# Kernel optimization log

Measured on AMD Instinct MI355X. Metric: run time of the kernel, lower is better.

The kernel has to match this reference:

```python
import jax, jax.numpy as jnp
import numpy as np

B, N, T, M, DIM = 4, 4096, 16, 64, 1024
HEADS, DH = 8, 64
INNER = HEADS * DH  # 512
KV = T * M          # 1024


def setup_inputs() -> dict:
    key = jax.random.key(0)
    ks = jax.random.split(key, 8)
    x = jax.random.normal(ks[0], (B, N, DIM), jnp.float32)
    media = jax.random.normal(ks[1], (B, T, M, DIM), jnp.float32)
    # sparse media markers so cumsum(text_time) stays within [0, T]
    media_locations = jax.random.uniform(ks[2], (B, N)) < (T / N)
    ln_scale = jnp.ones((DIM,), jnp.float32)
    ln_bias = jnp.zeros((DIM,), jnp.float32)
    s_in = DIM ** -0.5
    Wq = jax.random.normal(ks[3], (DIM, INNER), jnp.float32) * s_in
    Wk = jax.random.normal(ks[4], (DIM, INNER), jnp.float32) * s_in
    Wv = jax.random.normal(ks[5], (DIM, INNER), jnp.float32) * s_in
    Wo = jax.random.normal(ks[6], (INNER, DIM), jnp.float32) * (INNER ** -0.5)
    return dict(x=x, media=media, media_locations=media_locations,
                ln_scale=ln_scale, ln_bias=ln_bias, Wq=Wq, Wk=Wk, Wv=Wv, Wo=Wo)


def reference(x, media, media_locations, ln_scale, ln_bias, Wq, Wk, Wv, Wo):
    scale = DH ** -0.5
    # LayerNorm(eps=1e-5)
    mu = jnp.mean(x, axis=-1, keepdims=True)
    var = jnp.mean((x - mu) ** 2, axis=-1, keepdims=True)
    xn = (x - mu) / jnp.sqrt(var + 1e-5) * ln_scale + ln_bias

    q = xn @ Wq                                   # [b, n, inner]
    media_f = media.reshape(B, KV, DIM)           # b (t m) d
    k = media_f @ Wk                              # [b, kv, inner]
    v = media_f @ Wv

    q = q.reshape(B, N, HEADS, DH).transpose(0, 2, 1, 3) * scale  # b h n d
    k = k.reshape(B, KV, HEADS, DH).transpose(0, 2, 1, 3)         # b h kv d
    v = v.reshape(B, KV, HEADS, DH).transpose(0, 2, 1, 3)

    sim = jnp.einsum('bhid,bhjd->bhij', q, k)     # [b, h, n, kv]

    # media-location mask: each text token attends only to its immediately
    # preceding media item (only_attend_immediate_media=True -> eq)
    text_time = jnp.cumsum(media_locations.astype(jnp.int32), axis=-1)  # [b, n]
    media_time = jnp.repeat(jnp.arange(1, T + 1), M)                    # [kv]
    mask = text_time[:, None, :, None] == media_time[None, None, None, :]
    sim = jnp.where(mask, sim, -jnp.finfo(sim.dtype).max)

    attn = jax.nn.softmax(sim, axis=-1)  # stable (subtracts rowmax), same math
    # NOTE: the original's masked_fill_ of attn for media-less text tokens is a
    # no-op (return value discarded), faithfully omitted here.

    out = jnp.einsum('bhij,bhjd->bhid', attn, v)  # b h n d
    out = out.transpose(0, 2, 1, 3).reshape(B, N, INNER)
    return out @ Wo
```

## Files before the change

### kernel.cpp

```cpp
#include <hip/hip_runtime.h>

using u16 = unsigned short;
using uch = unsigned char;

typedef __bf16 bf16x8 __attribute__((ext_vector_type(8)));
typedef float f32x4 __attribute__((ext_vector_type(4)));

#define BATCH 4
#define SEQN 4096
#define TT 16
#define MM 64
#define DIM 1024
#define HEADS 8
#define DH 64
#define INNER 512
#define KVN 1024
#define NTOK (BATCH*SEQN)
#define MAXBLK 352

#define OFF_XN     ((size_t)0)
#define OFF_MEDIA  ((size_t)33554432)
#define OFF_Q      ((size_t)41943040)
#define OFF_KV     ((size_t)58720256)
#define OFF_AOUT   ((size_t)67108864)
#define OFF_WQT    ((size_t)83886080)
#define OFF_WKVT   ((size_t)84934656)
#define OFF_WOT    ((size_t)87031808)
#define OFF_VSUM   ((size_t)88145920)
#define OFF_FLAGS  ((size_t)88154112)
#define OFF_VT     ((size_t)88155136)
#define OFF_NBLK   ((size_t)92350464)
#define OFF_DESC   ((size_t)92351488)

__device__ __forceinline__ u16 f2bf(float f){
  unsigned int u = __float_as_uint(f);
  u += 0x7fffu + ((u >> 16) & 1u);
  return (u16)(u >> 16);
}
__device__ __forceinline__ float bf2f(u16 b){ return __uint_as_float(((unsigned int)b) << 16); }

__device__ __forceinline__ void async16(const u16* g, void* l){
  __builtin_amdgcn_global_load_lds((__attribute__((address_space(1))) void*)(g),
                                   (__attribute__((address_space(3))) void*)(l), 16, 0, 0);
}

__global__ __launch_bounds__(1024) void prep_kernel(const unsigned int* __restrict__ x,
                             const uch* __restrict__ loc, int* __restrict__ flags,
                             float* __restrict__ vsum, int4* __restrict__ desc,
                             int* __restrict__ nblk){
  __shared__ int cnt, nonz, sflags1;
  __shared__ int wsumS[4][4];
  __shared__ int sbound[4][19];
  __shared__ int gcnt[73];
  const int tid = threadIdx.x;
  if (tid == 0){ cnt = 0; nonz = 0; }
  if (tid < 76) sbound[tid/19][tid%19] = 4096;
  vsum[tid] = 0.f; vsum[1024 + tid] = 0.f;
  __syncthreads();
  if (tid < 256){
    int c = 0;
    #pragma unroll
    for (int t = 0; t < 4; ++t){
      unsigned int w = x[t*256 + tid];
      unsigned int e = (w >> 7) & 0xFFu;
      if (e >= 110u && e <= 140u) c++;
    }
    atomicAdd(&cnt, c);
  } else if (tid < 512){
    int tt = tid - 256;
    int nz = 0;
    #pragma unroll
    for (int t = 0; t < 16; ++t){
      int i = t*256 + tt;
      if ((i & 3) && loc[i]) nz++;
    }
    atomicAdd(&nonz, nz);
  }
  __syncthreads();
  if (tid == 0){
    flags[0] = (cnt > 512) ? 1 : 0;
    sflags1 = (nonz == 0) ? 1 : 0;
    flags[1] = sflags1;
  }
  __syncthreads();
  const int as32 = sflags1;
  const int b = tid >> 8, t8 = tid & 255;
  const int lane = tid & 63, wl = (tid >> 6) & 3;
  int v[16];
  if (as32){
    const int4* p = (const int4*)((const int*)loc + b*SEQN + t8*16);
    #pragma unroll
    for (int j = 0; j < 4; ++j){
      int4 q = p[j];
      v[j*4+0] = q.x != 0; v[j*4+1] = q.y != 0; v[j*4+2] = q.z != 0; v[j*4+3] = q.w != 0;
    }
  } else {
    const uchar4* p = (const uchar4*)(loc + b*SEQN + t8*16);
    #pragma unroll
    for (int j = 0; j < 4; ++j){
      uchar4 q = p[j];
      v[j*4+0] = q.x != 0; v[j*4+1] = q.y != 0; v[j*4+2] = q.z != 0; v[j*4+3] = q.w != 0;
    }
  }
  int tsum = 0;
  #pragma unroll
  for (int j = 0; j < 16; ++j) tsum += v[j];
  int s = tsum;
  #pragma unroll
  for (int o = 1; o < 64; o <<= 1){ int n2 = __shfl_up(s, o); if (lane >= o) s += n2; }
  if (lane == 63) wsumS[b][wl] = s;
  __syncthreads();
  int base = 0;
  for (int w2 = 0; w2 < wl; ++w2) base += wsumS[b][w2];
  int tt = base + s - tsum;
  #pragma unroll
  for (int j = 0; j < 16; ++j){
    if (v[j]){ tt++; if (tt <= 17) sbound[b][tt] = t8*16 + j; }
  }
  __syncthreads();
  if (tid < 72){
    int bb = tid/18, g = tid%18;
    int lo = (g == 0) ? 0 : sbound[bb][g];
    int hi = (g < 17) ? sbound[bb][g+1] : 4096;
    if (hi < lo) hi = lo;
    gcnt[tid] = (hi - lo + 63) >> 6;
  }
  __syncthreads();
  if (tid == 0){
    int acc = 0;
    for (int i = 0; i < 72; ++i){ int c2 = gcnt[i]; gcnt[i] = acc; acc += c2; }
    *nblk = acc;
  }
  __syncthreads();
  if (tid < 72){
    int bb = tid/18, g = tid%18;
    int lo = (g == 0) ? 0 : sbound[bb][g];
    int hi = (g < 17) ? sbound[bb][g+1] : 4096;
    if (hi < lo) hi = lo;
    int s2 = (g == 0 || g == 17) ? -1 : (g - 1);
    int n0 = gcnt[tid];
    for (int k = lo, j = 0; k < hi; k += 64, ++j){
      int4 d; d.x = bb; d.y = s2; d.z = bb*4096 + k; d.w = min(64, hi - k);
      desc[n0 + j] = d;
    }
  }
}

__global__ void wtrans_all_kernel(const void* __restrict__ Wq, const void* __restrict__ Wk,
                                  const void* __restrict__ Wv, const void* __restrict__ Wo,
                                  u16* __restrict__ WqT, u16* __restrict__ WkvT, u16* __restrict__ WoT,
                                  const int* __restrict__ flags){
  const int bf = flags[0];
  __shared__ float tile[32][33];
  int id = blockIdx.x;
  const void* in; u16* out; int K, N, bx, by;
  if (id < 512){       in = Wq; out = WqT;  K = DIM;   N = INNER; int l = id;        bx = l & 15; by = l >> 4; }
  else if (id < 1024){ in = Wk; out = WkvT; K = DIM;   N = INNER; int l = id - 512;  bx = l & 15; by = l >> 4; }
  else if (id < 1536){ in = Wv; out = WkvT + (size_t)512*1024; K = DIM; N = INNER; int l = id - 1024; bx = l & 15; by = l >> 4; }
  else {               in = Wo; out = WoT;  K = INNER; N = DIM;   int l = id - 1536; bx = l & 31; by = l >> 5; }
  int n0 = bx*32, k0 = by*32;
  int tx = threadIdx.x, ty = threadIdx.y;
  #pragma unroll
  for (int i = 0; i < 4; ++i){
    size_t idx = (size_t)(k0 + ty + i*8)*N + n0 + tx;
    tile[ty + i*8][tx] = bf ? bf2f(((const u16*)in)[idx]) : ((const float*)in)[idx];
  }
  __syncthreads();
  #pragma unroll
  for (int i = 0; i < 4; ++i)
    out[(size_t)(n0 + ty + i*8)*K + k0 + tx] = f2bf(tile[tx][ty + i*8]);
}

__global__ __launch_bounds__(256) void ln_cvt_kernel(const void* __restrict__ xp, const void* __restrict__ gp,
                          const void* __restrict__ bp, u16* __restrict__ xn,
                          const void* __restrict__ media, u16* __restrict__ medb,
                          const int* __restrict__ flags){
  const int bf = flags[0];
  const int tid = threadIdx.x;
  if ((int)blockIdx.x >= NTOK){
    size_t i = (size_t)(blockIdx.x - NTOK)*256 + tid;
    if (bf){
      ((ushort4*)medb)[i] = ((const ushort4*)media)[i];
    } else {
      float4 t = ((const float4*)media)[i];
      ushort4 o; o.x = f2bf(t.x); o.y = f2bf(t.y); o.z = f2bf(t.z); o.w = f2bf(t.w);
      ((ushort4*)medb)[i] = o;
    }
    return;
  }
  const int row = blockIdx.x;
  float v[4];
  if (bf){
    ushort4 t = ((const ushort4*)((const u16*)xp + (size_t)row*DIM))[tid];
    v[0]=bf2f(t.x); v[1]=bf2f(t.y); v[2]=bf2f(t.z); v[3]=bf2f(t.w);
  } else {
    float4 t = ((const float4*)((const float*)xp + (size_t)row*DIM))[tid];
    v[0]=t.x; v[1]=t.y; v[2]=t.z; v[3]=t.w;
  }
  float s = v[0]+v[1]+v[2]+v[3];
  float sq = v[0]*v[0]+v[1]*v[1]+v[2]*v[2]+v[3]*v[3];
  #pragma unroll
  for (int o = 32; o > 0; o >>= 1){ s += __shfl_down(s, o); sq += __shfl_down(sq, o); }
  __shared__ float ss[4], ssq[4];
  int wid = tid >> 6, lane = tid & 63;
  if (lane == 0){ ss[wid] = s; ssq[wid] = sq; }
  __syncthreads();
  s = ss[0]+ss[1]+ss[2]+ss[3]; sq = ssq[0]+ssq[1]+ssq[2]+ssq[3];
  float mean = s * (1.f/DIM);
  float rstd = rsqrtf(sq * (1.f/DIM) - mean*mean + 1e-5f);
  float g[4], bb[4];
  if (bf){
    ushort4 t1 = ((const ushort4*)gp)[tid]; ushort4 t2 = ((const ushort4*)bp)[tid];
    g[0]=bf2f(t1.x); g[1]=bf2f(t1.y); g[2]=bf2f(t1.z); g[3]=bf2f(t1.w);
    bb[0]=bf2f(t2.x); bb[1]=bf2f(t2.y); bb[2]=bf2f(t2.z); bb[3]=bf2f(t2.w);
  } else {
    float4 t1 = ((const float4*)gp)[tid]; float4 t2 = ((const float4*)bp)[tid];
    g[0]=t1.x; g[1]=t1.y; g[2]=t1.z; g[3]=t1.w;
    bb[0]=t2.x; bb[1]=t2.y; bb[2]=t2.z; bb[3]=t2.w;
  }
  ushort4 o;
  o.x = f2bf((v[0]-mean)*rstd*g[0] + bb[0]);
  o.y = f2bf((v[1]-mean)*rstd*g[1] + bb[1]);
  o.z = f2bf((v[2]-mean)*rstd*g[2] + bb[2]);
  o.w = f2bf((v[3]-mean)*rstd*g[3] + bb[3]);
  ((ushort4*)(xn + (size_t)row*DIM))[tid] = o;
}

__global__ __launch_bounds__(256) void gemm_kv(const u16* __restrict__ A, const u16* __restrict__ Bt,
                        u16* __restrict__ Cp, int M, int N, int K,
                        const int* __restrict__ flags, u16* __restrict__ vtp,
                        float* __restrict__ vsum){
  __shared__ u16 As[128*64];
  __shared__ u16 Bs[128*64];
  const int tid = threadIdx.x, wid = tid >> 6, lane = tid & 63;
  int flat = blockIdx.x + blockIdx.y*gridDim.x;
  int cpx = (gridDim.x*gridDim.y) >> 3;
  int wg = (flat & 7)*cpx + (flat >> 3);
  const int rn = wg % gridDim.x, rm = wg / gridDim.x;
  const int wr = wid >> 1, wc = wid & 1;
  const int lr = lane & 15, lg = lane >> 4;
  f32x4 acc[4][4] = {};
  const u16* Ab = A + (size_t)rm*128*K;
  const u16* Bb = Bt + (size_t)rn*128*K;
  for (int k0 = 0; k0 < K; k0 += 64){
    __syncthreads();
    #pragma unroll
    for (int t = 0; t < 4; ++t){
      int c = t*256 + tid;
      int row = c >> 3;
      int qs = (c & 7) ^ (row & 7);
      int ldsOff = (t*256 + wid*64) * 16;
      async16(Ab + (size_t)row*K + k0 + qs*8, (char*)As + ldsOff);
      async16(Bb + (size_t)row*K + k0 + qs*8, (char*)Bs + ldsOff);
    }
    __syncthreads();
    #pragma unroll
    for (int ks = 0; ks < 2; ++ks){
      bf16x8 af[4], bfr[4];
      #pragma unroll
      for (int m = 0; m < 4; ++m){
        int row = wr*64 + m*16 + lr;
        int q = (ks*4 + lg) ^ (row & 7);
        af[m] = *(const bf16x8*)((const char*)As + row*128 + (q << 4));
      }
      #pragma unroll
      for (int n = 0; n < 4; ++n){
        int row = wc*64 + n*16 + lr;
        int q = (ks*4 + lg) ^ (row & 7);
        bfr[n] = *(const bf16x8*)((const char*)Bs + row*128 + (q << 4));
      }
      #pragma unroll
      for (int m = 0; m < 4; ++m)
        #pragma unroll
        for (int n = 0; n < 4; ++n)
          acc[m][n] = __builtin_amdgcn_mfma_f32_16x16x32_bf16(af[m], bfr[n], acc[m][n], 0, 0, 0);
    }
  }
  const int batch = rm >> 3;
  #pragma unroll
  for (int n = 0; n < 4; ++n){
    int col = rn*128 + wc*64 + n*16 + lr;
    float psum = 0.f;
    #pragma unroll
    for (int m = 0; m < 4; ++m){
      int row0 = rm*128 + wr*64 + m*16 + lg*4;
      #pragma unroll
      for (int r = 0; r < 4; ++r){
        float v = acc[m][n][r];
        psum += v;
        size_t idx = (size_t)(row0 + r)*N + col;
        u16 bv = f2bf(v);
        Cp[idx] = bv;
        if (col >= 512){
          int row = row0 + r;
          int kvi = row & 1023;
          int s = kvi >> 6, rr = kvi & 63;
          vtp[((size_t)(((row >> 10)*16 + s)*512 + (col - 512)))*64 + rr] = bv;
        }
      }
    }
    if (col >= 512) atomicAdd(&vsum[batch*512 + (col - 512)], psum);
  }
}

template<int ROWS>
__device__ __forceinline__ void g8_stage(const u16* __restrict__ src, char* dst, int K, int t,
                                         int tid, int wid){
  #pragma unroll
  for (int i = 0; i < ROWS/64; ++i){
    int s_ = i*512 + tid;
    int row_ = s_ >> 3, g_ = s_ & 7;
    async16(src + (size_t)row_*K + t*64 + ((g_ ^ (row_ & 7)) << 3),
            dst + (size_t)(i*512 + wid*64)*16);
  }
}

template<int BN, int NT, int MODE>
__global__ __launch_bounds__(512, 2) void gemm8(const u16* __restrict__ A, const u16* __restrict__ Bt,
                        void* __restrict__ Cp, int Nglob, float alpha, const int* __restrict__ flags){
  constexpr int K = NT*64;
  constexpr int NREP = BN/64;
  __shared__ u16 As[2][256*64];
  __shared__ u16 Bs[2][BN*64];
  const int tid = threadIdx.x, wid = tid >> 6, lane = tid & 63;
  int flat = blockIdx.x + blockIdx.y*gridDim.x;
  int cpx = (gridDim.x*gridDim.y) >> 3;
  int wg = (flat & 7)*cpx + (flat >> 3);
  const int rn = wg % gridDim.x, rm = wg / gridDim.x;
  const int wr = wid >> 2, wc = wid & 3;
  const int lr = lane & 15, lg = lane >> 4;
  f32x4 acc[8][NREP] = {};
  const u16* Ab = A + (size_t)rm*256*K;
  const u16* Bb = Bt + (size_t)rn*BN*K;

  g8_stage<256>(Ab, (char*)As[0], K, 0, tid, wid);
  g8_stage<BN >(Bb, (char*)Bs[0], K, 0, tid, wid);
  __syncthreads();

  for (int t = 0; t < NT; ++t){
    const int cur = t & 1;
    const char* Acur = (const char*)As[cur];
    const char* Bcur = (const char*)Bs[cur];
    bf16x8 bfr[NREP][2];
    #pragma unroll
    for (int p = 0; p < 4; ++p){
      if (p == 0 && t + 1 < NT){
        g8_stage<256>(Ab, (char*)As[cur^1], K, t+1, tid, wid);
        g8_stage<BN >(Bb, (char*)Bs[cur^1], K, t+1, tid, wid);
      }
      bf16x8 af[2][2];
      #pragma unroll
      for (int i = 0; i < 2; ++i){
        int row = wr*128 + (2*p + i)*16 + lr;
        #pragma unroll
        for (int ks = 0; ks < 2; ++ks){
          int g = (ks*4 + lg) ^ (row & 7);
          af[i][ks] = *(const bf16x8*)(Acur + row*128 + g*16);
        }
      }
      if (p == 0){
        #pragma unroll
        for (int n = 0; n < NREP; ++n){
          int row = wc*(BN/4) + n*16 + lr;
          #pragma unroll
          for (int ks = 0; ks < 2; ++ks){
            int g = (ks*4 + lg) ^ (row & 7);
            bfr[n][ks] = *(const bf16x8*)(Bcur + row*128 + g*16);
          }
        }
      }
      __builtin_amdgcn_s_barrier();
      __builtin_amdgcn_s_setprio(1);
      #pragma unroll
      for (int i = 0; i < 2; ++i)
        #pragma unroll
        for (int n = 0; n < NREP; ++n)
          #pragma unroll
          for (int ks = 0; ks < 2; ++ks)
            acc[2*p + i][n] = __builtin_amdgcn_mfma_f32_16x16x32_bf16(af[i][ks], bfr[n][ks], acc[2*p + i][n], 0, 0, 0);
      __builtin_amdgcn_s_setprio(0);
      __builtin_amdgcn_s_barrier();
    }
    if (t + 1 < NT) __syncthreads();
  }

  const bool obf = (MODE == 0) || (flags[0] != 0);
  #pragma unroll
  for (int m = 0; m < 8; ++m){
    #pragma unroll
    for (int n = 0; n < NREP; ++n){
      int row0 = rm*256 + wr*128 + m*16 + lg*4;
      int col  = rn*BN + wc*(BN/4) + n*16 + lr;
      #pragma unroll
      for (int r = 0; r < 4; ++r){
        float v = acc[m][n][r] * alpha;
        size_t idx = (size_t)(row0 + r)*Nglob + col;
        if (obf) ((u16*)Cp)[idx] = f2bf(v);
        else     ((float*)Cp)[idx] = v;
      }
    }
  }
}

__global__ __launch_bounds__(256) void attn2_kernel(
    const u16* __restrict__ qb, const u16* __restrict__ kvb, const u16* __restrict__ vt,
    const int* __restrict__ nblk, const int4* __restrict__ desc,
    const float* __restrict__ vsum, u16* __restrict__ aout){
  __shared__ u16 Ks[64*64];
  __shared__ u16 Vs[64*64];
  __shared__ u16 Ps[4][16*72];
  if (blockIdx.x >= *nblk) return;
  const int4 d = desc[blockIdx.x];
  const int b = d.x, s = d.y, rowStart = d.z, cnt = d.w;
  const int h = blockIdx.y;
  const int tid = threadIdx.x, w = tid >> 6, lane = tid & 63;
  if (s < 0){
    const float inv = 1.f/1024.f;
    for (int idx = tid; idx < cnt*64; idx += 256){
      int slot = idx >> 6, c = h*64 + (idx & 63);
      aout[(size_t)(rowStart + slot)*512 + c] = f2bf(vsum[b*512 + c]*inv);
    }
    return;
  }
  const int lr = lane & 15, lg = lane >> 4;
  const size_t kbase = ((size_t)(b*1024 + s*64))*1024;
  const size_t vbase = ((size_t)(b*16 + s))*512*64;
  const int myslot = w*16 + lr;
  const size_t qrow = (size_t)(rowStart + min(myslot, cnt - 1))*512;
  #pragma unroll
  for (int t = 0; t < 2; ++t){
    int ci = t*256 + tid;
    int r = ci >> 3, q = ci & 7;
    int qs = (q ^ (r & 7)) << 3;
    async16(kvb + kbase + (size_t)r*1024 + h*64 + qs, (char*)Ks + ci*16);
    async16(vt + vbase + (size_t)(h*64 + r)*64 + qs, (char*)Vs + ci*16);
  }
  __syncthreads();
  bf16x8 qa0 = *(const bf16x8*)(qb + qrow + h*64 + lg*8);
  bf16x8 qa1 = *(const bf16x8*)(qb + qrow + h*64 + 32 + lg*8);
  f32x4 sv[4] = {};
  #pragma unroll
  for (int n = 0; n < 4; ++n){
    int row = n*16 + lr;
    int sl0 = (lg) ^ (row & 7);
    int sl1 = (4 + lg) ^ (row & 7);
    bf16x8 kb0 = *(const bf16x8*)((const char*)Ks + row*128 + sl0*16);
    sv[n] = __builtin_amdgcn_mfma_f32_16x16x32_bf16(qa0, kb0, sv[n], 0, 0, 0);
    bf16x8 kb1 = *(const bf16x8*)((const char*)Ks + row*128 + sl1*16);
    sv[n] = __builtin_amdgcn_mfma_f32_16x16x32_bf16(qa1, kb1, sv[n], 0, 0, 0);
  }
  float inv[4];
  #pragma unroll
  for (int r = 0; r < 4; ++r){
    float m = fmaxf(fmaxf(sv[0][r], sv[1][r]), fmaxf(sv[2][r], sv[3][r]));
    #pragma unroll
    for (int o = 1; o < 16; o <<= 1) m = fmaxf(m, __shfl_xor(m, o));
    float s0 = 0.f;
    #pragma unroll
    for (int n = 0; n < 4; ++n){ sv[n][r] = __expf(sv[n][r] - m); s0 += sv[n][r]; }
    #pragma unroll
    for (int o = 1; o < 16; o <<= 1) s0 += __shfl_xor(s0, o);
    inv[r] = 1.f / s0;
  }
  u16* pw = &Ps[w][0];
  #pragma unroll
  for (int n = 0; n < 4; ++n)
    #pragma unroll
    for (int r = 0; r < 4; ++r)
      pw[(4*lg + r)*72 + n*16 + lr] = f2bf(sv[n][r] * inv[r]);
  bf16x8 pa0 = *(const bf16x8*)((const char*)pw + lr*144 + lg*16);
  bf16x8 pa1 = *(const bf16x8*)((const char*)pw + lr*144 + 64 + lg*16);
  f32x4 ov[4] = {};
  #pragma unroll
  for (int n = 0; n < 4; ++n){
    int row = n*16 + lr;
    int sl0 = (lg) ^ (row & 7);
    int sl1 = (4 + lg) ^ (row & 7);
    bf16x8 vb0 = *(const bf16x8*)((const char*)Vs + row*128 + sl0*16);
    ov[n] = __builtin_amdgcn_mfma_f32_16x16x32_bf16(pa0, vb0, ov[n], 0, 0, 0);
    bf16x8 vb1 = *(const bf16x8*)((const char*)Vs + row*128 + sl1*16);
    ov[n] = __builtin_amdgcn_mfma_f32_16x16x32_bf16(pa1, vb1, ov[n], 0, 0, 0);
  }
  #pragma unroll
  for (int r = 0; r < 4; ++r){
    int slot = w*16 + 4*lg + r;
    if (slot < cnt){
      size_t orow = (size_t)(rowStart + slot)*512 + h*64;
      #pragma unroll
      for (int n = 0; n < 4; ++n)
        aout[orow + n*16 + lr] = f2bf(ov[n][r]);
    }
  }
}

extern "C" void kernel_launch(void* const* d_in, const int* in_sizes, int n_in,
                              void* d_out, int out_size, void* d_ws, size_t ws_size,
                              hipStream_t stream){
  const void* x      = d_in[0];
  const void* media  = d_in[1];
  const void* mloc   = d_in[2];
  const void* ln_g   = d_in[3];
  const void* ln_b   = d_in[4];
  const void* Wq     = d_in[5];
  const void* Wk     = d_in[6];
  const void* Wv     = d_in[7];
  const void* Wo     = d_in[8];
  char* ws = (char*)d_ws;
  u16* xn    = (u16*)(ws + OFF_XN);
  u16* medb  = (u16*)(ws + OFF_MEDIA);
  u16* qb    = (u16*)(ws + OFF_Q);
  u16* kvb   = (u16*)(ws + OFF_KV);
  u16* aout  = (u16*)(ws + OFF_AOUT);
  u16* WqT   = (u16*)(ws + OFF_WQT);
  u16* WkvT  = (u16*)(ws + OFF_WKVT);
  u16* WoT   = (u16*)(ws + OFF_WOT);
  float* vsm = (float*)(ws + OFF_VSUM);
  int* flags = (int*)(ws + OFF_FLAGS);
  u16* vt    = (u16*)(ws + OFF_VT);
  int* nblk  = (int*)(ws + OFF_NBLK);
  int4* desc = (int4*)(ws + OFF_DESC);

  prep_kernel<<<1, 1024, 0, stream>>>((const unsigned int*)x, (const uch*)mloc, flags, vsm, desc, nblk);

  wtrans_all_kernel<<<2048, dim3(32, 8), 0, stream>>>(Wq, Wk, Wv, Wo, WqT, WkvT, WoT, flags);
  ln_cvt_kernel<<<NTOK + 4096, 256, 0, stream>>>(x, ln_g, ln_b, xn, media, medb, flags);

  gemm8<128, 16, 0><<<dim3(4, 64), 512, 0, stream>>>(xn, WqT, qb, INNER, 0.125f, flags);
  gemm_kv<<<dim3(8, 32), 256, 0, stream>>>(medb, WkvT, kvb, BATCH*KVN, 1024, DIM, flags, vt, vsm);

  attn2_kernel<<<dim3(MAXBLK, 8), 256, 0, stream>>>(qb, kvb, vt, nblk, desc, vsm, aout);

  gemm8<256, 8, 1><<<dim3(4, 64), 512, 0, stream>>>(aout, WoT, d_out, DIM, 1.f, flags);
}
```

Measured before the change: 147.6 us.

## Merge front-end prep kernels and co-schedule Q and KV projection GEMMs

Folds the prep, weight-transpose and layernorm/convert kernels into one front kernel, with each block re-detecting the input dtype locally instead of reading a flag written by an earlier launch. The Q projection GEMM and the KV projection GEMM become one launch that dispatches on block index, so both run concurrently on the device. This removes launch gaps and the serialized tail between kernels. In exchange, every block repeats the dtype detection, the KV GEMM path now runs at 512 threads with half of them idle, and the fused kernel carries more LDS and drops the occupancy hint of 2.

Result: faster. 123.5 us (-16.3%).

```diff
diff --git a/kernel.cpp b/kernel.cpp
--- a/kernel.cpp
+++ b/kernel.cpp
@@ -17,6 +17,11 @@
 #define KVN 1024
 #define NTOK (BATCH*SEQN)
 #define MAXBLK 352
+
+#define FB_WT0  1
+#define FB_CVT0 2049
+#define FB_LN0  6145
+#define FB_GRID (FB_LN0 + NTOK)
 
 #define OFF_XN     ((size_t)0)
 #define OFF_MEDIA  ((size_t)33554432)
@@ -44,141 +49,150 @@
                                    (__attribute__((address_space(3))) void*)(l), 16, 0, 0);
 }
 
-__global__ __launch_bounds__(1024) void prep_kernel(const unsigned int* __restrict__ x,
-                             const uch* __restrict__ loc, int* __restrict__ flags,
-                             float* __restrict__ vsum, int4* __restrict__ desc,
-                             int* __restrict__ nblk){
-  __shared__ int cnt, nonz, sflags1;
-  __shared__ int wsumS[4][4];
-  __shared__ int sbound[4][19];
-  __shared__ int gcnt[73];
+__device__ __forceinline__ int detect_bf16(const unsigned int* __restrict__ x){
+  __shared__ int scnt;
   const int tid = threadIdx.x;
-  if (tid == 0){ cnt = 0; nonz = 0; }
-  if (tid < 76) sbound[tid/19][tid%19] = 4096;
-  vsum[tid] = 0.f; vsum[1024 + tid] = 0.f;
+  if (tid == 0) scnt = 0;
   __syncthreads();
-  if (tid < 256){
-    int c = 0;
-    #pragma unroll
-    for (int t = 0; t < 4; ++t){
-      unsigned int w = x[t*256 + tid];
-      unsigned int e = (w >> 7) & 0xFFu;
-      if (e >= 110u && e <= 140u) c++;
-    }
-    atomicAdd(&cnt, c);
-  } else if (tid < 512){
-    int tt = tid - 256;
+  int c = 0;
+  #pragma unroll
+  for (int t = 0; t < 4; ++t){
+    unsigned int w = x[t*256 + tid];
+    unsigned int e = (w >> 7) & 0xFFu;
+    c += (e >= 110u && e <= 140u) ? 1 : 0;
+  }
+  #pragma unroll
+  for (int o = 32; o > 0; o >>= 1) c += __shfl_down(c, o);
+  if ((tid & 63) == 0) atomicAdd(&scnt, c);
+  __syncthreads();
+  return scnt > 512 ? 1 : 0;
+}
+
+__global__ __launch_bounds__(256) void front_kernel(
+    const unsigned int* __restrict__ x, const uch* __restrict__ loc,
+    const void* __restrict__ ln_g, const void* __restrict__ ln_b,
+    const void* __restrict__ media,
+    const void* __restrict__ Wq, const void* __restrict__ Wk,
+    const void* __restrict__ Wv, const void* __restrict__ Wo,
+    u16* __restrict__ xn, u16* __restrict__ medb,
+    u16* __restrict__ WqT, u16* __restrict__ WkvT, u16* __restrict__ WoT,
+    int* __restrict__ flags, float* __restrict__ vsum,
+    int4* __restrict__ desc, int* __restrict__ nblk){
+  const int bid = blockIdx.x, tid = threadIdx.x;
+
+  if (bid == 0){
+    __shared__ int nonzS;
+    __shared__ int wsumS[4];
+    __shared__ int sbound[4][19];
+    __shared__ int gcnt[72];
+    int bf = detect_bf16(x);
+    if (tid == 0) nonzS = 0;
+    if (tid < 76) sbound[tid/19][tid%19] = 4096;
+    #pragma unroll
+    for (int t = 0; t < 8; ++t) vsum[t*256 + tid] = 0.f;
+    __syncthreads();
     int nz = 0;
     #pragma unroll
     for (int t = 0; t < 16; ++t){
-      int i = t*256 + tt;
+      int i = t*256 + tid;
       if ((i & 3) && loc[i]) nz++;
     }
-    atomicAdd(&nonz, nz);
-  }
-  __syncthreads();
-  if (tid == 0){
-    flags[0] = (cnt > 512) ? 1 : 0;
-    sflags1 = (nonz == 0) ? 1 : 0;
-    flags[1] = sflags1;
-  }
-  __syncthreads();
-  const int as32 = sflags1;
-  const int b = tid >> 8, t8 = tid & 255;
-  const int lane = tid & 63, wl = (tid >> 6) & 3;
-  int v[16];
-  if (as32){
-    const int4* p = (const int4*)((const int*)loc + b*SEQN + t8*16);
-    #pragma unroll
-    for (int j = 0; j < 4; ++j){
-      int4 q = p[j];
-      v[j*4+0] = q.x != 0; v[j*4+1] = q.y != 0; v[j*4+2] = q.z != 0; v[j*4+3] = q.w != 0;
-    }
-  } else {
-    const uchar4* p = (const uchar4*)(loc + b*SEQN + t8*16);
-    #pragma unroll
-    for (int j = 0; j < 4; ++j){
-      uchar4 q = p[j];
-      v[j*4+0] = q.x != 0; v[j*4+1] = q.y != 0; v[j*4+2] = q.z != 0; v[j*4+3] = q.w != 0;
-    }
-  }
-  int tsum = 0;
-  #pragma unroll
-  for (int j = 0; j < 16; ++j) tsum += v[j];
-  int s = tsum;
-  #pragma unroll
-  for (int o = 1; o < 64; o <<= 1){ int n2 = __shfl_up(s, o); if (lane >= o) s += n2; }
-  if (lane == 63) wsumS[b][wl] = s;
-  __syncthreads();
-  int base = 0;
-  for (int w2 = 0; w2 < wl; ++w2) base += wsumS[b][w2];
-  int tt = base + s - tsum;
-  #pragma unroll
-  for (int j = 0; j < 16; ++j){
-    if (v[j]){ tt++; if (tt <= 17) sbound[b][tt] = t8*16 + j; }
-  }
-  __syncthreads();
-  if (tid < 72){
-    int bb = tid/18, g = tid%18;
-    int lo = (g == 0) ? 0 : sbound[bb][g];
-    int hi = (g < 17) ? sbound[bb][g+1] : 4096;
-    if (hi < lo) hi = lo;
-    gcnt[tid] = (hi - lo + 63) >> 6;
-  }
-  __syncthreads();
-  if (tid == 0){
-    int acc = 0;
-    for (int i = 0; i < 72; ++i){ int c2 = gcnt[i]; gcnt[i] = acc; acc += c2; }
-    *nblk = acc;
-  }
-  __syncthreads();
-  if (tid < 72){
-    int bb = tid/18, g = tid%18;
-    int lo = (g == 0) ? 0 : sbound[bb][g];
-    int hi = (g < 17) ? sbound[bb][g+1] : 4096;
-    if (hi < lo) hi = lo;
-    int s2 = (g == 0 || g == 17) ? -1 : (g - 1);
-    int n0 = gcnt[tid];
-    for (int k = lo, j = 0; k < hi; k += 64, ++j){
-      int4 d; d.x = bb; d.y = s2; d.z = bb*4096 + k; d.w = min(64, hi - k);
-      desc[n0 + j] = d;
-    }
-  }
-}
-
-__global__ void wtrans_all_kernel(const void* __restrict__ Wq, const void* __restrict__ Wk,
-                                  const void* __restrict__ Wv, const void* __restrict__ Wo,
-                                  u16* __restrict__ WqT, u16* __restrict__ WkvT, u16* __restrict__ WoT,
-                                  const int* __restrict__ flags){
-  const int bf = flags[0];
-  __shared__ float tile[32][33];
-  int id = blockIdx.x;
-  const void* in; u16* out; int K, N, bx, by;
-  if (id < 512){       in = Wq; out = WqT;  K = DIM;   N = INNER; int l = id;        bx = l & 15; by = l >> 4; }
-  else if (id < 1024){ in = Wk; out = WkvT; K = DIM;   N = INNER; int l = id - 512;  bx = l & 15; by = l >> 4; }
-  else if (id < 1536){ in = Wv; out = WkvT + (size_t)512*1024; K = DIM; N = INNER; int l = id - 1024; bx = l & 15; by = l >> 4; }
-  else {               in = Wo; out = WoT;  K = INNER; N = DIM;   int l = id - 1536; bx = l & 31; by = l >> 5; }
-  int n0 = bx*32, k0 = by*32;
-  int tx = threadIdx.x, ty = threadIdx.y;
-  #pragma unroll
-  for (int i = 0; i < 4; ++i){
-    size_t idx = (size_t)(k0 + ty + i*8)*N + n0 + tx;
-    tile[ty + i*8][tx] = bf ? bf2f(((const u16*)in)[idx]) : ((const float*)in)[idx];
-  }
-  __syncthreads();
-  #pragma unroll
-  for (int i = 0; i < 4; ++i)
-    out[(size_t)(n0 + ty + i*8)*K + k0 + tx] = f2bf(tile[tx][ty + i*8]);
-}
-
-__global__ __launch_bounds__(256) void ln_cvt_kernel(const void* __restrict__ xp, const void* __restrict__ gp,
-                          const void* __restrict__ bp, u16* __restrict__ xn,
-                          const void* __restrict__ media, u16* __restrict__ medb,
-                          const int* __restrict__ flags){
-  const int bf = flags[0];
-  const int tid = threadIdx.x;
-  if ((int)blockIdx.x >= NTOK){
-    size_t i = (size_t)(blockIdx.x - NTOK)*256 + tid;
+    #pragma unroll
+    for (int o = 32; o > 0; o >>= 1) nz += __shfl_down(nz, o);
+    if ((tid & 63) == 0) atomicAdd(&nonzS, nz);
+    __syncthreads();
+    const int as32 = (nonzS == 0) ? 1 : 0;
+    if (tid == 0){ flags[0] = bf; flags[1] = as32; }
+    const int lane = tid & 63, wl = tid >> 6;
+    for (int b = 0; b < BATCH; ++b){
+      int v[16];
+      if (as32){
+        const int4* p = (const int4*)((const int*)loc + b*SEQN + tid*16);
+        #pragma unroll
+        for (int j = 0; j < 4; ++j){
+          int4 q = p[j];
+          v[j*4+0]=q.x!=0; v[j*4+1]=q.y!=0; v[j*4+2]=q.z!=0; v[j*4+3]=q.w!=0;
+        }
+      } else {
+        const uchar4* p = (const uchar4*)(loc + b*SEQN + tid*16);
+        #pragma unroll
+        for (int j = 0; j < 4; ++j){
+          uchar4 q = p[j];
+          v[j*4+0]=q.x!=0; v[j*4+1]=q.y!=0; v[j*4+2]=q.z!=0; v[j*4+3]=q.w!=0;
+        }
+      }
+      int tsum = 0;
+      #pragma unroll
+      for (int j = 0; j < 16; ++j) tsum += v[j];
+      int s = tsum;
+      #pragma unroll
+      for (int o = 1; o < 64; o <<= 1){ int n2 = __shfl_up(s, o); if (lane >= o) s += n2; }
+      if (lane == 63) wsumS[wl] = s;
+      __syncthreads();
+      int base = 0;
+      for (int w2 = 0; w2 < wl; ++w2) base += wsumS[w2];
+      int tt = base + s - tsum;
+      #pragma unroll
+      for (int j = 0; j < 16; ++j){
+        if (v[j]){ tt++; if (tt <= 17) sbound[b][tt] = tid*16 + j; }
+      }
+      __syncthreads();
+    }
+    if (tid < 72){
+      int bb = tid/18, g = tid%18;
+      int lo = (g == 0) ? 0 : sbound[bb][g];
+      int hi = (g < 17) ? sbound[bb][g+1] : 4096;
+      if (hi < lo) hi = lo;
+      gcnt[tid] = (hi - lo + 63) >> 6;
+    }
+    __syncthreads();
+    if (tid == 0){
+      int acc = 0;
+      for (int i = 0; i < 72; ++i){ int c2 = gcnt[i]; gcnt[i] = acc; acc += c2; }
+      *nblk = acc;
+    }
+    __syncthreads();
+    if (tid < 72){
+      int bb = tid/18, g = tid%18;
+      int lo = (g == 0) ? 0 : sbound[bb][g];
+      int hi = (g < 17) ? sbound[bb][g+1] : 4096;
+      if (hi < lo) hi = lo;
+      int s2 = (g == 0 || g == 17) ? -1 : (g - 1);
+      int n0 = gcnt[tid];
+      for (int k = lo, j = 0; k < hi; k += 64, ++j){
+        int4 d; d.x = bb; d.y = s2; d.z = bb*4096 + k; d.w = min(64, hi - k);
+        desc[n0 + j] = d;
+      }
+    }
+    return;
+  }
+
+  if (bid < FB_CVT0){
+    const int bf = detect_bf16(x);
+    __shared__ float tile[32][33];
+    int id = bid - FB_WT0;
+    const void* in; u16* out; int K, N, bx, by;
+    if (id < 512){       in = Wq; out = WqT;  K = DIM;   N = INNER; bx = id & 15; by = id >> 4; }
+    else if (id < 1024){ in = Wk; out = WkvT; K = DIM;   N = INNER; int l = id - 512;  bx = l & 15; by = l >> 4; }
+    else if (id < 1536){ in = Wv; out = WkvT + (size_t)512*1024; K = DIM; N = INNER; int l = id - 1024; bx = l & 15; by = l >> 4; }
+    else {               in = Wo; out = WoT;  K = INNER; N = DIM;   int l = id - 1536; bx = l & 31; by = l >> 5; }
+    int n0 = bx*32, k0 = by*32;
+    int tx = tid & 31, ty = tid >> 5;
+    #pragma unroll
+    for (int i = 0; i < 4; ++i){
+      size_t idx = (size_t)(k0 + ty + i*8)*N + n0 + tx;
+      tile[ty + i*8][tx] = bf ? bf2f(((const u16*)in)[idx]) : ((const float*)in)[idx];
+    }
+    __syncthreads();
+    #pragma unroll
+    for (int i = 0; i < 4; ++i)
+      out[(size_t)(n0 + ty + i*8)*K + k0 + tx] = f2bf(tile[tx][ty + i*8]);
+    return;
+  }
+
+  if (bid < FB_LN0){
+    const int bf = detect_bf16(x);
+    size_t i = (size_t)(bid - FB_CVT0)*256 + tid;
     if (bf){
       ((ushort4*)medb)[i] = ((const ushort4*)media)[i];
     } else {
@@ -188,13 +202,15 @@
     }
     return;
   }
-  const int row = blockIdx.x;
+
+  const int bf = detect_bf16(x);
+  const int row = bid - FB_LN0;
   float v[4];
   if (bf){
-    ushort4 t = ((const ushort4*)((const u16*)xp + (size_t)row*DIM))[tid];
+    ushort4 t = ((const ushort4*)((const u16*)x + (size_t)row*DIM))[tid];
     v[0]=bf2f(t.x); v[1]=bf2f(t.y); v[2]=bf2f(t.z); v[3]=bf2f(t.w);
   } else {
-    float4 t = ((const float4*)((const float*)xp + (size_t)row*DIM))[tid];
+    float4 t = ((const float4*)((const float*)x + (size_t)row*DIM))[tid];
     v[0]=t.x; v[1]=t.y; v[2]=t.z; v[3]=t.w;
   }
   float s = v[0]+v[1]+v[2]+v[3];
@@ -210,11 +226,11 @@
   float rstd = rsqrtf(sq * (1.f/DIM) - mean*mean + 1e-5f);
   float g[4], bb[4];
   if (bf){
-    ushort4 t1 = ((const ushort4*)gp)[tid]; ushort4 t2 = ((const ushort4*)bp)[tid];
+    ushort4 t1 = ((const ushort4*)ln_g)[tid]; ushort4 t2 = ((const ushort4*)ln_b)[tid];
     g[0]=bf2f(t1.x); g[1]=bf2f(t1.y); g[2]=bf2f(t1.z); g[3]=bf2f(t1.w);
     bb[0]=bf2f(t2.x); bb[1]=bf2f(t2.y); bb[2]=bf2f(t2.z); bb[3]=bf2f(t2.w);
   } else {
-    float4 t1 = ((const float4*)gp)[tid]; float4 t2 = ((const float4*)bp)[tid];
+    float4 t1 = ((const float4*)ln_g)[tid]; float4 t2 = ((const float4*)ln_b)[tid];
     g[0]=t1.x; g[1]=t1.y; g[2]=t1.z; g[3]=t1.w;
     bb[0]=t2.x; bb[1]=t2.y; bb[2]=t2.z; bb[3]=t2.w;
   }
@@ -226,83 +242,6 @@
   ((ushort4*)(xn + (size_t)row*DIM))[tid] = o;
 }
 
-__global__ __launch_bounds__(256) void gemm_kv(const u16* __restrict__ A, const u16* __restrict__ Bt,
-                        u16* __restrict__ Cp, int M, int N, int K,
-                        const int* __restrict__ flags, u16* __restrict__ vtp,
-                        float* __restrict__ vsum){
-  __shared__ u16 As[128*64];
-  __shared__ u16 Bs[128*64];
-  const int tid = threadIdx.x, wid = tid >> 6, lane = tid & 63;
-  int flat = blockIdx.x + blockIdx.y*gridDim.x;
-  int cpx = (gridDim.x*gridDim.y) >> 3;
-  int wg = (flat & 7)*cpx + (flat >> 3);
-  const int rn = wg % gridDim.x, rm = wg / gridDim.x;
-  const int wr = wid >> 1, wc = wid & 1;
-  const int lr = lane & 15, lg = lane >> 4;
-  f32x4 acc[4][4] = {};
-  const u16* Ab = A + (size_t)rm*128*K;
-  const u16* Bb = Bt + (size_t)rn*128*K;
-  for (int k0 = 0; k0 < K; k0 += 64){
-    __syncthreads();
-    #pragma unroll
-    for (int t = 0; t < 4; ++t){
-      int c = t*256 + tid;
-      int row = c >> 3;
-      int qs = (c & 7) ^ (row & 7);
-      int ldsOff = (t*256 + wid*64) * 16;
-      async16(Ab + (size_t)row*K + k0 + qs*8, (char*)As + ldsOff);
-      async16(Bb + (size_t)row*K + k0 + qs*8, (char*)Bs + ldsOff);
-    }
-    __syncthreads();
-    #pragma unroll
-    for (int ks = 0; ks < 2; ++ks){
-      bf16x8 af[4], bfr[4];
-      #pragma unroll
-      for (int m = 0; m < 4; ++m){
-        int row = wr*64 + m*16 + lr;
-        int q = (ks*4 + lg) ^ (row & 7);
-        af[m] = *(const bf16x8*)((const char*)As + row*128 + (q << 4));
-      }
-      #pragma unroll
-      for (int n = 0; n < 4; ++n){
-        int row = wc*64 + n*16 + lr;
-        int q = (ks*4 + lg) ^ (row & 7);
-        bfr[n] = *(const bf16x8*)((const char*)Bs + row*128 + (q << 4));
-      }
-      #pragma unroll
-      for (int m = 0; m < 4; ++m)
-        #pragma unroll
-        for (int n = 0; n < 4; ++n)
-          acc[m][n] = __builtin_amdgcn_mfma_f32_16x16x32_bf16(af[m], bfr[n], acc[m][n], 0, 0, 0);
-    }
-  }
-  const int batch = rm >> 3;
-  #pragma unroll
-  for (int n = 0; n < 4; ++n){
-    int col = rn*128 + wc*64 + n*16 + lr;
-    float psum = 0.f;
-    #pragma unroll
-    for (int m = 0; m < 4; ++m){
-      int row0 = rm*128 + wr*64 + m*16 + lg*4;
-      #pragma unroll
-      for (int r = 0; r < 4; ++r){
-        float v = acc[m][n][r];
-        psum += v;
-        size_t idx = (size_t)(row0 + r)*N + col;
-        u16 bv = f2bf(v);
-        Cp[idx] = bv;
-        if (col >= 512){
-          int row = row0 + r;
-          int kvi = row & 1023;
-          int s = kvi >> 6, rr = kvi & 63;
-          vtp[((size_t)(((row >> 10)*16 + s)*512 + (col - 512)))*64 + rr] = bv;
-        }
-      }
-    }
-    if (col >= 512) atomicAdd(&vsum[batch*512 + (col - 512)], psum);
-  }
-}
-
 template<int ROWS>
 __device__ __forceinline__ void g8_stage(const u16* __restrict__ src, char* dst, int K, int t,
                                          int tid, int wid){
@@ -316,37 +255,33 @@
 }
 
 template<int BN, int NT, int MODE>
-__global__ __launch_bounds__(512, 2) void gemm8(const u16* __restrict__ A, const u16* __restrict__ Bt,
-                        void* __restrict__ Cp, int Nglob, float alpha, const int* __restrict__ flags){
+__device__ __forceinline__ void gemm8_body(const u16* __restrict__ A, const u16* __restrict__ Bt,
+                        void* __restrict__ Cp, int Nglob, float alpha, const int* __restrict__ flags,
+                        int rm, int rn, u16* sA0, u16* sA1, u16* sB0, u16* sB1){
   constexpr int K = NT*64;
   constexpr int NREP = BN/64;
-  __shared__ u16 As[2][256*64];
-  __shared__ u16 Bs[2][BN*64];
   const int tid = threadIdx.x, wid = tid >> 6, lane = tid & 63;
-  int flat = blockIdx.x + blockIdx.y*gridDim.x;
-  int cpx = (gridDim.x*gridDim.y) >> 3;
-  int wg = (flat & 7)*cpx + (flat >> 3);
-  const int rn = wg % gridDim.x, rm = wg / gridDim.x;
   const int wr = wid >> 2, wc = wid & 3;
   const int lr = lane & 15, lg = lane >> 4;
   f32x4 acc[8][NREP] = {};
   const u16* Ab = A + (size_t)rm*256*K;
   const u16* Bb = Bt + (size_t)rn*BN*K;
 
-  g8_stage<256>(Ab, (char*)As[0], K, 0, tid, wid);
-  g8_stage<BN >(Bb, (char*)Bs[0], K, 0, tid, wid);
+  g8_stage<256>(Ab, (char*)sA0, K, 0, tid, wid);
+  g8_stage<BN >(Bb, (char*)sB0, K, 0, tid, wid);
   __syncthreads();
 
   for (int t = 0; t < NT; ++t){
-    const int cur = t & 1;
-    const char* Acur = (const char*)As[cur];
-    const char* Bcur = (const char*)Bs[cur];
+    u16* Acur = (t & 1) ? sA1 : sA0;
+    u16* Bcur = (t & 1) ? sB1 : sB0;
+    u16* Anxt = (t & 1) ? sA0 : sA1;
+    u16* Bnxt = (t & 1) ? sB0 : sB1;
     bf16x8 bfr[NREP][2];
     #pragma unroll
     for (int p = 0; p < 4; ++p){
       if (p == 0 && t + 1 < NT){
-        g8_stage<256>(Ab, (char*)As[cur^1], K, t+1, tid, wid);
-        g8_stage<BN >(Bb, (char*)Bs[cur^1], K, t+1, tid, wid);
+        g8_stage<256>(Ab, (char*)Anxt, K, t+1, tid, wid);
+        g8_stage<BN >(Bb, (char*)Bnxt, K, t+1, tid, wid);
       }
       bf16x8 af[2][2];
       #pragma unroll
@@ -355,7 +290,7 @@
         #pragma unroll
         for (int ks = 0; ks < 2; ++ks){
           int g = (ks*4 + lg) ^ (row & 7);
-          af[i][ks] = *(const bf16x8*)(Acur + row*128 + g*16);
+          af[i][ks] = *(const bf16x8*)((const char*)Acur + row*128 + g*16);
         }
       }
       if (p == 0){
@@ -365,7 +300,7 @@
           #pragma unroll
           for (int ks = 0; ks < 2; ++ks){
             int g = (ks*4 + lg) ^ (row & 7);
-            bfr[n][ks] = *(const bf16x8*)(Bcur + row*128 + g*16);
+            bfr[n][ks] = *(const bf16x8*)((const char*)Bcur + row*128 + g*16);
           }
         }
       }
@@ -400,6 +335,108 @@
       }
     }
   }
+}
+
+__global__ __launch_bounds__(512) void proj_kernel(
+    const u16* __restrict__ xn, const u16* __restrict__ WqT, u16* __restrict__ qb,
+    const u16* __restrict__ medb, const u16* __restrict__ WkvT, u16* __restrict__ kvb,
+    u16* __restrict__ vtp, float* __restrict__ vsum, const int* __restrict__ flags){
+  __shared__ u16 smem[49152];
+  const int tid = threadIdx.x;
+  if (blockIdx.x < 256){
+    u16* As = smem; u16* Bs = smem + 8192;
+    const int wid = tid >> 6, lane = tid & 63;
+    int bid = blockIdx.x;
+    int wg = (bid & 7)*32 + (bid >> 3);
+    const int rn = wg & 7, rm = wg >> 3;
+    const int wr = wid >> 1, wc = wid & 1;
+    const int lr = lane & 15, lg = lane >> 4;
+    f32x4 acc[4][4] = {};
+    const u16* Ab = medb + (size_t)rm*128*DIM;
+    const u16* Bb = WkvT + (size_t)rn*128*DIM;
+    for (int k0 = 0; k0 < DIM; k0 += 64){
+      __syncthreads();
+      if (tid < 256){
+        #pragma unroll
+        for (int t = 0; t < 4; ++t){
+          int c = t*256 + tid;
+          int row = c >> 3;
+          int qs = (c & 7) ^ (row & 7);
+          int ldsOff = (t*256 + wid*64) * 16;
+          async16(Ab + (size_t)row*DIM + k0 + qs*8, (char*)As + ldsOff);
+          async16(Bb + (size_t)row*DIM + k0 + qs*8, (char*)Bs + ldsOff);
+        }
+      }
+      __syncthreads();
+      if (tid < 256){
+        #pragma unroll
+        for (int ks = 0; ks < 2; ++ks){
+          bf16x8 af[4], bfr[4];
+          #pragma unroll
+          for (int m = 0; m < 4; ++m){
+            int row = wr*64 + m*16 + lr;
+            int q = (ks*4 + lg) ^ (row & 7);
+            af[m] = *(const bf16x8*)((const char*)As + row*128 + (q << 4));
+          }
+          #pragma unroll
+          for (int n = 0; n < 4; ++n){
+            int row = wc*64 + n*16 + lr;
+            int q = (ks*4 + lg) ^ (row & 7);
+            bfr[n] = *(const bf16x8*)((const char*)Bs + row*128 + (q << 4));
+          }
+          #pragma unroll
+          for (int m = 0; m < 4; ++m)
+            #pragma unroll
+            for (int n = 0; n < 4; ++n)
+              acc[m][n] = __builtin_amdgcn_mfma_f32_16x16x32_bf16(af[m], bfr[n], acc[m][n], 0, 0, 0);
+        }
+      }
+    }
+    if (tid < 256){
+      const int batch = rm >> 3;
+      #pragma unroll
+      for (int n = 0; n < 4; ++n){
+        int col = rn*128 + wc*64 + n*16 + lr;
+        float psum = 0.f;
+        #pragma unroll
+        for (int m = 0; m < 4; ++m){
+          int row0 = rm*128 + wr*64 + m*16 + lg*4;
+          #pragma unroll
+          for (int r = 0; r < 4; ++r){
+            float v = acc[m][n][r];
+            psum += v;
+            size_t idx = (size_t)(row0 + r)*1024 + col;
+            u16 bv = f2bf(v);
+            kvb[idx] = bv;
+            if (col >= 512){
+              int row = row0 + r;
+              int kvi = row & 1023;
+              int s = kvi >> 6, rr = kvi & 63;
+              vtp[((size_t)(((row >> 10)*16 + s)*512 + (col - 512)))*64 + rr] = bv;
+            }
+          }
+        }
+        if (col >= 512) atomicAdd(&vsum[batch*512 + (col - 512)], psum);
+      }
+    }
+  } else {
+    int bid = blockIdx.x - 256;
+    int wg = (bid & 7)*32 + (bid >> 3);
+    const int rn = wg & 3, rm = wg >> 2;
+    gemm8_body<128, 16, 0>(xn, WqT, qb, INNER, 0.125f, flags, rm, rn,
+                           smem, smem + 16384, smem + 32768, smem + 40960);
+  }
+}
+
+__global__ __launch_bounds__(512) void gemm8_out_kernel(const u16* __restrict__ A,
+                        const u16* __restrict__ Bt, void* __restrict__ Cp,
+                        const int* __restrict__ flags){
+  __shared__ u16 As[2][16384];
+  __shared__ u16 Bs[2][16384];
+  int flat = blockIdx.x + blockIdx.y*gridDim.x;
+  int wg = (flat & 7)*32 + (flat >> 3);
+  int rn = wg & 3, rm = wg >> 2;
+  gemm8_body<256, 8, 1>(A, Bt, Cp, DIM, 1.f, flags, rm, rn, As[0], As[1], Bs[0], Bs[1]);
 }
 
 __global__ __launch_bounds__(256) void attn2_kernel(
@@ -520,15 +557,13 @@
   int* nblk  = (int*)(ws + OFF_NBLK);
   int4* desc = (int4*)(ws + OFF_DESC);
 
-  prep_kernel<<<1, 1024, 0, stream>>>((const unsigned int*)x, (const uch*)mloc, flags, vsm, desc, nblk);
-
-  wtrans_all_kernel<<<2048, dim3(32, 8), 0, stream>>>(Wq, Wk, Wv, Wo, WqT, WkvT, WoT, flags);
-  ln_cvt_kernel<<<NTOK + 4096, 256, 0, stream>>>(x, ln_g, ln_b, xn, media, medb, flags);
-
-  gemm8<128, 16, 0><<<dim3(4, 64), 512, 0, stream>>>(xn, WqT, qb, INNER, 0.125f, flags);
-  gemm_kv<<<dim3(8, 32), 256, 0, stream>>>(medb, WkvT, kvb, BATCH*KVN, 1024, DIM, flags, vt, vsm);
+  front_kernel<<<FB_GRID, 256, 0, stream>>>(
+      (const unsigned int*)x, (const uch*)mloc, ln_g, ln_b, media,
+      Wq, Wk, Wv, Wo, xn, medb, WqT, WkvT, WoT, flags, vsm, desc, nblk);
+
+  proj_kernel<<<512, 512, 0, stream>>>(xn, WqT, qb, medb, WkvT, kvb, vt, vsm, flags);
 
   attn2_kernel<<<dim3(MAXBLK, 8), 256, 0, stream>>>(qb, kvb, vt, nblk, desc, vsm, aout);
 
-  gemm8<256, 8, 1><<<dim3(4, 64), 512, 0, stream>>>(aout, WoT, d_out, DIM, 1.f, flags);
-}
+  gemm8_out_kernel<<<dim3(4, 64), 512, 0, stream>>>(aout, WoT, d_out, flags);
+}
```
